# Kernel optimization log

Hardware: AMD Instinct MI355X
Metric: run time of the kernel (lower is better)

## Reference

```python
import jax, jax.numpy as jnp
import numpy as np

N, E, B = 30000, 360000, 8
FN, FE, D, L, M = 64, 16, 128, 3, 8
DK = D // M
NEG_SLOPE = 0.2
EPS = 1e-5


def setup_inputs() -> dict:
    key = jax.random.key(0)
    ks = jax.random.split(key, 24)
    rng = np.random.default_rng(0)
    Ng, Eg = N // B, E // B
    off = np.repeat(np.arange(B, dtype=np.int64) * Ng, Eg)
    src = jnp.asarray(rng.integers(0, Ng, size=E) + off, dtype=jnp.int32)
    dst = jnp.asarray(rng.integers(0, Ng, size=E) + off, dtype=jnp.int32)
    node_graph = jnp.asarray(np.repeat(np.arange(B), Ng), dtype=jnp.int32)
    edge_graph = jnp.asarray(np.repeat(np.arange(B), Eg), dtype=jnp.int32)
    p = lambda i, *s: jax.random.normal(ks[i], s, jnp.float32) * 0.05
    return dict(
        h=jax.random.normal(ks[0], (N, FN), jnp.float32),
        e=jax.random.normal(ks[1], (E, FE), jnp.float32),
        src=src, dst=dst, node_graph=node_graph, edge_graph=edge_graph,
        emb_n_w=p(2, D, FN), emb_n_b=p(3, D),
        emb_e_w=p(4, D, FE), emb_e_b=p(5, D),
        Us=p(6, L, D, D), Vs=p(7, L, D, D), As=p(8, L, D, D),
        Bs=p(9, L, D, D), Cs=p(10, L, D, D),
        gat_src_w=p(11, M * DK, D), gat_src_b=p(12, M * DK),
        gat_dst_w=p(13, M * DK, D), gat_dst_b=p(14, M * DK),
        gat_attn=p(15, M, DK), gat_bias=p(16, M * DK),
        O_w=p(17, D, D), O_b=p(18, D),
        W1_w=p(19, D, 3 * D), W1_b=p(20, D),
        W2_w=p(21, 1, D), W2_b=p(22, 1))


def _bn(x):
    # BatchNorm1d(affine=False), training mode: biased variance over batch dim
    return (x - x.mean(0)) * jax.lax.rsqrt(x.var(0) + EPS)


def reference(h, e, src, dst, node_graph, edge_graph,
              emb_n_w, emb_n_b, emb_e_w, emb_e_b,
              Us, Vs, As, Bs, Cs,
              gat_src_w, gat_src_b, gat_dst_w, gat_dst_b, gat_attn, gat_bias,
              O_w, O_b, W1_w, W1_b, W2_w, W2_b):
    h = h @ emb_n_w.T + emb_n_b  # [N, D]
    e = e @ emb_e_w.T + emb_e_b  # [E, D]
    for l in range(L):
        # u_mul_e('h','w','m') + max('m','agg'): gather-mul-segment_max
        m = (h @ Vs[l].T)[src] * jax.nn.sigmoid(e)  # [E, D]
        agg = jax.ops.segment_max(m, dst, num_segments=N)
        agg = jnp.where(jnp.isneginf(agg), 0.0, agg)  # DGL fills zero-in-degree with 0
        h_new = h + jax.nn.relu(_bn(h @ Us[l].T + agg))
        # inc('in')^T @ B(h) = B(h)[dst]; inc('out')^T @ C(h) = C(h)[src] (uses pre-update h)
        ee = (h @ Bs[l].T)[dst] + (h @ Cs[l].T)[src]
        e = e + jax.nn.relu(_bn(e @ As[l].T + ee))
        h = h_new
    # GATv2Conv(D, DK, M heads, allow_zero_in_degree=True)
    fs = (h @ gat_src_w.T + gat_src_b).reshape(N, M, DK)
    fd = (h @ gat_dst_w.T + gat_dst_b).reshape(N, M, DK)
    z = jax.nn.leaky_relu(fs[src] + fd[dst], NEG_SLOPE)  # [E, M, DK]
    score = jnp.einsum('emk,mk->em', z, gat_attn)        # [E, M]
    smax = jax.ops.segment_max(score, dst, num_segments=N)[dst]
    p = jnp.exp(score - smax)
    denom = jax.ops.segment_sum(p, dst, num_segments=N)[dst]
    a = p / denom
    rst = jax.ops.segment_sum(a[:, :, None] * fs[src], dst, num_segments=N)
    rst = rst + gat_bias.reshape(1, M, DK)
    h = rst.reshape(N, D) @ O_w.T + O_b
    # per-graph mean of node states, broadcast to that graph's edges
    cnt = jax.ops.segment_sum(jnp.ones((N,), h.dtype), node_graph, num_segments=B)
    moy = jax.ops.segment_sum(h, node_graph, num_segments=B) / cnt[:, None]
    out = jnp.concatenate([moy[edge_graph], h[src], h[dst]], axis=1)  # [E, 3D]
    out = jax.nn.relu(out @ W1_w.T + W1_b)
    out = out @ W2_w.T + W2_b
    return jax.nn.sigmoid(out)[:, 0]
```

## Files before the change

kernel.cpp:

```cpp
#include <hip/hip_runtime.h>

#define DF 128
#define NGRAPH 8

typedef __attribute__((ext_vector_type(8))) short bf16x8;
typedef __attribute__((ext_vector_type(4))) float f32x4;

__device__ __forceinline__ float sigm(float x) { return 1.f / (1.f + __expf(-x)); }
__device__ __forceinline__ unsigned short f2bf(float f) {
  unsigned u = __float_as_uint(f);
  u += 0x7FFFu + ((u >> 16) & 1u);
  return (unsigned short)(u >> 16);
}
__device__ __forceinline__ float bf2f(unsigned short u) {
  return __uint_as_float(((unsigned)u) << 16);
}
__device__ __forceinline__ float bflo(unsigned u) { return __uint_as_float(u << 16); }
__device__ __forceinline__ float bfhi(unsigned u) { return __uint_as_float(u & 0xffff0000u); }

__device__ __forceinline__ bf16x8 cvt8(const float* __restrict__ p) {
  float4 a = *(const float4*)p;
  float4 b = *(const float4*)(p + 4);
  bf16x8 r;
  r[0] = (short)f2bf(a.x); r[1] = (short)f2bf(a.y);
  r[2] = (short)f2bf(a.z); r[3] = (short)f2bf(a.w);
  r[4] = (short)f2bf(b.x); r[5] = (short)f2bf(b.y);
  r[6] = (short)f2bf(b.z); r[7] = (short)f2bf(b.w);
  return r;
}

__device__ __forceinline__ void agg_max(unsigned hv, unsigned ev, float& m0, float& m1) {
  m0 = fmaxf(m0, bflo(hv) * sigm(bflo(ev)));
  m1 = fmaxf(m1, bfhi(hv) * sigm(bfhi(ev)));
}

__global__ void k_fill_u32(unsigned* __restrict__ p, unsigned v, long long n) {
  long long i = (long long)blockIdx.x * blockDim.x + threadIdx.x;
  long long st = (long long)gridDim.x * blockDim.x;
  for (; i < n; i += st) p[i] = v;
}

__global__ void k_deg(const int* __restrict__ dst, unsigned* __restrict__ deg, int E) {
  int i = blockIdx.x * blockDim.x + threadIdx.x;
  int st = gridDim.x * blockDim.x;
  for (; i < E; i += st) atomicAdd(&deg[dst[i]], 1u);
}

__global__ __launch_bounds__(1024) void k_scan(
    const unsigned* __restrict__ deg, unsigned* __restrict__ rowptr,
    unsigned* __restrict__ cursor, int N) {
  __shared__ unsigned part[1024];
  int t = threadIdx.x;
  int per = (N + 1023) >> 10;
  int s0 = t * per, s1 = min(N, s0 + per);
  unsigned s = 0;
  for (int i = s0; i < s1; ++i) s += deg[i];
  part[t] = s;
  __syncthreads();
  for (int off = 1; off < 1024; off <<= 1) {
    unsigned v = (t >= off) ? part[t - off] : 0u;
    __syncthreads();
    part[t] += v;
    __syncthreads();
  }
  unsigned base = (t == 0) ? 0u : part[t - 1];
  for (int i = s0; i < s1; ++i) {
    rowptr[i] = base;
    cursor[i] = base;
    base += deg[i];
  }
  if (t == 1023) rowptr[N] = part[1023];
}

__global__ void k_scatter(const int* __restrict__ dst, unsigned* __restrict__ cursor,
                          int* __restrict__ eidb, int E) {
  int i = blockIdx.x * blockDim.x + threadIdx.x;
  int st = gridDim.x * blockDim.x;
  for (; i < E; i += st) {
    unsigned p = atomicAdd(&cursor[dst[i]], 1u);
    eidb[p] = i;
  }
}

__global__ void k_permidx(const int* __restrict__ eidb, const int* __restrict__ src,
                          const int* __restrict__ dst, int* __restrict__ srcP,
                          int* __restrict__ dstP, int E) {
  int i = blockIdx.x * blockDim.x + threadIdx.x;
  int st = gridDim.x * blockDim.x;
  for (; i < E; i += st) {
    int e = eidb[i];
    srcP[i] = src[e];
    dstP[i] = dst[e];
  }
}

__global__ __launch_bounds__(512) void k_wconv(
    const float* __restrict__ Us, const float* __restrict__ Vs,
    const float* __restrict__ As, const float* __restrict__ Bs,
    const float* __restrict__ Cs, const float* __restrict__ gsw,
    const float* __restrict__ gdw, const float* __restrict__ Ow,
    const float* __restrict__ W1, short* __restrict__ out) {
  int b = blockIdx.x;
  const float* W;
  int ldw = DF;
  if (b < 3) W = Us + b * 16384;
  else if (b < 6) W = Vs + (b - 3) * 16384;
  else if (b < 9) W = As + (b - 6) * 16384;
  else if (b < 12) W = Bs + (b - 9) * 16384;
  else if (b < 15) W = Cs + (b - 12) * 16384;
  else if (b == 15) W = gsw;
  else if (b == 16) W = gdw;
  else if (b == 17) W = Ow;
  else if (b == 18) { W = W1 + 128; ldw = 384; }
  else { W = W1 + 256; ldw = 384; }
  short* o = out + (size_t)b * 2048 * 8;
  for (int s = threadIdx.x; s < 2048; s += 512) {
    int ct = s >> 8, ks = (s >> 6) & 3, l = s & 63;
    int row = ct * 16 + (l & 15), k0 = ks * 32 + (l >> 4) * 8;
    *(bf16x8*)&o[s * 8] = cvt8(W + (size_t)row * ldw + k0);
  }
}

__global__ __launch_bounds__(128) void k_node_embed(
    const float* __restrict__ hin, const float* __restrict__ w,
    const float* __restrict__ b, float* __restrict__ h0, int rows) {
  __shared__ float Wt[64 * DF];
  __shared__ float ar[4][64];
  int tid = threadIdx.x;
  for (int i = tid; i < 64 * DF; i += 128) Wt[(i & 63) * DF + (i >> 6)] = w[i];
  float bb = b[tid];
  __syncthreads();
  for (int r0 = blockIdx.x * 4; r0 < rows; r0 += gridDim.x * 4) {
    for (int i = tid; i < 256; i += 128) ar[i >> 6][i & 63] = hin[(size_t)r0 * 64 + i];
    __syncthreads();
    float a0 = bb, a1 = bb, a2 = bb, a3 = bb;
#pragma unroll 8
    for (int k = 0; k < 64; ++k) {
      float wv = Wt[k * DF + tid];
      a0 = fmaf(ar[0][k], wv, a0); a1 = fmaf(ar[1][k], wv, a1);
      a2 = fmaf(ar[2][k], wv, a2); a3 = fmaf(ar[3][k], wv, a3);
    }
    h0[(size_t)r0 * DF + tid] = a0;
    h0[(size_t)(r0 + 1) * DF + tid] = a1;
    h0[(size_t)(r0 + 2) * DF + tid] = a2;
    h0[(size_t)(r0 + 3) * DF + tid] = a3;
    __syncthreads();
  }
}

__global__ __launch_bounds__(128) void k_edge_embed(
    const float* __restrict__ ein, const int* __restrict__ eidb,
    const float* __restrict__ w, const float* __restrict__ b,
    unsigned short* __restrict__ e0u, int rows) {
  __shared__ float Wt[16 * DF];
  __shared__ float ar[4][16];
  int tid = threadIdx.x;
  for (int i = tid; i < 16 * DF; i += 128) Wt[(i & 15) * DF + (i >> 4)] = w[i];
  float bb = b[tid];
  __syncthreads();
  for (int r0 = blockIdx.x * 4; r0 < rows; r0 += gridDim.x * 4) {
    if (tid < 64) {
      int e = eidb[r0 + (tid >> 4)];
      ar[tid >> 4][tid & 15] = ein[(size_t)e * 16 + (tid & 15)];
    }
    __syncthreads();
    float a0 = bb, a1 = bb, a2 = bb, a3 = bb;
#pragma unroll
    for (int k = 0; k < 16; ++k) {
      float wv = Wt[k * DF + tid];
      a0 = fmaf(ar[0][k], wv, a0); a1 = fmaf(ar[1][k], wv, a1);
      a2 = fmaf(ar[2][k], wv, a2); a3 = fmaf(ar[3][k], wv, a3);
    }
    e0u[(size_t)r0 * DF + tid] = f2bf(a0);
    e0u[(size_t)(r0 + 1) * DF + tid] = f2bf(a1);
    e0u[(size_t)(r0 + 2) * DF + tid] = f2bf(a2);
    e0u[(size_t)(r0 + 3) * DF + tid] = f2bf(a3);
    __syncthreads();
  }
}

template <int OUTBF>
__global__ __launch_bounds__(512) void k_gemm_mfma(
    const float* __restrict__ A, const short* __restrict__ Wf,
    const float* __restrict__ bias, void* __restrict__ outv, int rows) {
  __shared__ short Wb[2048 * 8];
  int tid = threadIdx.x;
  for (int s = tid; s < 2048; s += 512)
    *(bf16x8*)&Wb[s * 8] = *(const bf16x8*)&Wf[(size_t)s * 8];
  __syncthreads();
  float* outf = (float*)outv;
  unsigned short* outb = (unsigned short*)outv;
  int wid = tid >> 6, lane = tid & 63, q = lane >> 4, m = lane & 15;
  int ntiles = (rows + 127) >> 7;
  for (int t = blockIdx.x; t < ntiles; t += gridDim.x) {
    int r0 = t * 128 + wid * 16;
    int rr = r0 + m;
    if (rr >= rows) rr = rows - 1;
    const float* ap = A + (size_t)rr * DF + q * 8;
    bf16x8 a[4];
#pragma unroll
    for (int ks = 0; ks < 4; ++ks) a[ks] = cvt8(ap + 32 * ks);
#pragma unroll
    for (int ct = 0; ct < 8; ++ct) {
      f32x4 acc = {0.f, 0.f, 0.f, 0.f};
#pragma unroll
      for (int ks = 0; ks < 4; ++ks) {
        bf16x8 b = *(const bf16x8*)&Wb[((ct * 4 + ks) * 64 + lane) * 8];
        acc = __builtin_amdgcn_mfma_f32_16x16x32_bf16(a[ks], b, acc, 0, 0, 0);
      }
      int col = ct * 16 + m;
      float bb = bias ? bias[col] : 0.f;
#pragma unroll
      for (int j = 0; j < 4; ++j) {
        int row = r0 + q * 4 + j;
        if (row < rows) {
          if (OUTBF) outb[(size_t)row * DF + col] = f2bf(acc[j] + bb);
          else outf[(size_t)row * DF + col] = acc[j] + bb;
        }
      }
    }
  }
}

__global__ __launch_bounds__(512) void k_gemmb_mfma(
    const unsigned short* __restrict__ A, const short* __restrict__ Wf,
    unsigned short* __restrict__ outb, int rows) {
  __shared__ short Wb[2048 * 8];
  int tid = threadIdx.x;
  for (int s = tid; s < 2048; s += 512)
    *(bf16x8*)&Wb[s * 8] = *(const bf16x8*)&Wf[(size_t)s * 8];
  __syncthreads();
  int wid = tid >> 6, lane = tid & 63, q = lane >> 4, m = lane & 15;
  int ntiles = (rows + 127) >> 7;
  for (int t = blockIdx.x; t < ntiles; t += gridDim.x) {
    int r0 = t * 128 + wid * 16;
    int rr = r0 + m;
    if (rr >= rows) rr = rows - 1;
    const unsigned short* ap = A + (size_t)rr * DF + q * 8;
    bf16x8 a[4];
#pragma unroll
    for (int ks = 0; ks < 4; ++ks) a[ks] = *(const bf16x8*)(ap + 32 * ks);
#pragma unroll
    for (int ct = 0; ct < 8; ++ct) {
      f32x4 acc = {0.f, 0.f, 0.f, 0.f};
#pragma unroll
      for (int ks = 0; ks < 4; ++ks) {
        bf16x8 b = *(const bf16x8*)&Wb[((ct * 4 + ks) * 64 + lane) * 8];
        acc = __builtin_amdgcn_mfma_f32_16x16x32_bf16(a[ks], b, acc, 0, 0, 0);
      }
      int col = ct * 16 + m;
#pragma unroll
      for (int j = 0; j < 4; ++j) {
        int row = r0 + q * 4 + j;
        if (row < rows) outb[(size_t)row * DF + col] = f2bf(acc[j]);
      }
    }
  }
}

__global__ __launch_bounds__(512) void k_gemm4_mfma(
    const float* __restrict__ h0, const short* __restrict__ Vf,
    const short* __restrict__ Uf, const short* __restrict__ Bf,
    const short* __restrict__ Cf, unsigned short* __restrict__ hVb,
    float* __restrict__ hU, unsigned short* __restrict__ hBb,
    unsigned short* __restrict__ hCb, int rows) {
  __shared__ short Wl[4 * 2048 * 8];
  int tid = threadIdx.x;
  for (int s = tid; s < 2048; s += 512) {
    *(bf16x8*)&Wl[(size_t)s * 8] = *(const bf16x8*)&Vf[(size_t)s * 8];
    *(bf16x8*)&Wl[(size_t)(2048 + s) * 8] = *(const bf16x8*)&Uf[(size_t)s * 8];
    *(bf16x8*)&Wl[(size_t)(4096 + s) * 8] = *(const bf16x8*)&Bf[(size_t)s * 8];
    *(bf16x8*)&Wl[(size_t)(6144 + s) * 8] = *(const bf16x8*)&Cf[(size_t)s * 8];
  }
  __syncthreads();
  int wid = tid >> 6, lane = tid & 63, q = lane >> 4, m = lane & 15;
  int ntiles = (rows + 127) >> 7;
  for (int t = blockIdx.x; t < ntiles; t += gridDim.x) {
    int r0 = t * 128 + wid * 16;
    int rr = r0 + m;
    if (rr >= rows) rr = rows - 1;
    const float* ap = h0 + (size_t)rr * DF + q * 8;
    bf16x8 a[4];
#pragma unroll
    for (int ks = 0; ks < 4; ++ks) a[ks] = cvt8(ap + 32 * ks);
#pragma unroll
    for (int w = 0; w < 4; ++w) {
#pragma unroll
      for (int ct = 0; ct < 8; ++ct) {
        f32x4 acc = {0.f, 0.f, 0.f, 0.f};
#pragma unroll
        for (int ks = 0; ks < 4; ++ks) {
          bf16x8 b = *(const bf16x8*)&Wl[((w * 2048) + (ct * 4 + ks) * 64 + lane) * 8];
          acc = __builtin_amdgcn_mfma_f32_16x16x32_bf16(a[ks], b, acc, 0, 0, 0);
        }
        int col = ct * 16 + m;
#pragma unroll
        for (int j = 0; j < 4; ++j) {
          int row = r0 + q * 4 + j;
          if (row < rows) {
            if (w == 1) hU[(size_t)row * DF + col] = acc[j];
            else {
              unsigned short v = f2bf(acc[j]);
              unsigned short* o = (w == 0) ? hVb : ((w == 2) ? hBb : hCb);
              o[(size_t)row * DF + col] = v;
            }
          }
        }
      }
    }
  }
}

#define EDGE_MFMA_BODY                                                                 \
  const unsigned short* ep = e0u + (size_t)ec * DF + q * 8;                            \
  bf16x8 bv0 = *(const bf16x8*)(ep);                                                   \
  bf16x8 bv1 = *(const bf16x8*)(ep + 32);                                              \
  bf16x8 bv2 = *(const bf16x8*)(ep + 64);                                              \
  bf16x8 bv3 = *(const bf16x8*)(ep + 96);                                              \
  f32x4 c0 = {0.f, 0.f, 0.f, 0.f}, c1 = c0, c2 = c0, c3 = c0;                          \
  f32x4 c4 = c0, c5 = c0, c6 = c0, c7 = c0;                                            \
  _Pragma("unroll") for (int ks = 0; ks < 4; ++ks) {                                   \
    bf16x8 bv = (ks == 0) ? bv0 : (ks == 1) ? bv1 : (ks == 2) ? bv2 : bv3;             \
    c0 = __builtin_amdgcn_mfma_f32_16x16x32_bf16(*(const bf16x8*)&Wb[((0 * 4 + ks) * 64 + lane) * 8], bv, c0, 0, 0, 0); \
    c1 = __builtin_amdgcn_mfma_f32_16x16x32_bf16(*(const bf16x8*)&Wb[((1 * 4 + ks) * 64 + lane) * 8], bv, c1, 0, 0, 0); \
    c2 = __builtin_amdgcn_mfma_f32_16x16x32_bf16(*(const bf16x8*)&Wb[((2 * 4 + ks) * 64 + lane) * 8], bv, c2, 0, 0, 0); \
    c3 = __builtin_amdgcn_mfma_f32_16x16x32_bf16(*(const bf16x8*)&Wb[((3 * 4 + ks) * 64 + lane) * 8], bv, c3, 0, 0, 0); \
    c4 = __builtin_amdgcn_mfma_f32_16x16x32_bf16(*(const bf16x8*)&Wb[((4 * 4 + ks) * 64 + lane) * 8], bv, c4, 0, 0, 0); \
    c5 = __builtin_amdgcn_mfma_f32_16x16x32_bf16(*(const bf16x8*)&Wb[((5 * 4 + ks) * 64 + lane) * 8], bv, c5, 0, 0, 0); \
    c6 = __builtin_amdgcn_mfma_f32_16x16x32_bf16(*(const bf16x8*)&Wb[((6 * 4 + ks) * 64 + lane) * 8], bv, c6, 0, 0, 0); \
    c7 = __builtin_amdgcn_mfma_f32_16x16x32_bf16(*(const bf16x8*)&Wb[((7 * 4 + ks) * 64 + lane) * 8], bv, c7, 0, 0, 0); \
  }

__global__ __launch_bounds__(512) void k_edge_xs(
    const unsigned short* __restrict__ e0u, const short* __restrict__ Af,
    const unsigned short* __restrict__ hBb, const unsigned short* __restrict__ hCb,
    const int* __restrict__ srcP, const int* __restrict__ dstP,
    float* __restrict__ stat, int Eg) {
  __shared__ short Wb[2048 * 8];
  __shared__ float ls[256];
  int tid = threadIdx.x;
  for (int s = tid; s < 2048; s += 512)
    *(bf16x8*)&Wb[s * 8] = *(const bf16x8*)&Af[(size_t)s * 8];
  if (tid < 256) ls[tid] = 0.f;
  int wid = tid >> 6, lane = tid & 63, q = lane >> 4, m = lane & 15;
  int g = blockIdx.x & 7, sub = blockIdx.x >> 3, nsub = gridDim.x >> 3;
  int gbase = g * Eg, gend = gbase + Eg;
  int tpg = (Eg + 127) >> 7;
  float ps[32], pq[32];
#pragma unroll
  for (int i = 0; i < 32; ++i) { ps[i] = 0.f; pq[i] = 0.f; }
  __syncthreads();
  for (int t = sub; t < tpg; t += nsub) {
    int r0 = gbase + t * 128 + wid * 16;
    int edge = r0 + m;
    bool ok = edge < gend;
    int ec = ok ? edge : gend - 1;
    EDGE_MFMA_BODY
    if (ok) {
      int sidx = srcP[ec], didx = dstP[ec];
      const unsigned short* pb = hBb + (size_t)didx * DF + q * 4;
      const unsigned short* pc = hCb + (size_t)sidx * DF + q * 4;
#pragma unroll
      for (int ct = 0; ct < 8; ++ct) {
        f32x4 cc = (ct == 0) ? c0 : (ct == 1) ? c1 : (ct == 2) ? c2 : (ct == 3) ? c3
                   : (ct == 4) ? c4 : (ct == 5) ? c5 : (ct == 6) ? c6 : c7;
        ushort4 hb = *(const ushort4*)(pb + ct * 16);
        ushort4 hc = *(const ushort4*)(pc + ct * 16);
        float x0 = cc[0] + bf2f(hb.x) + bf2f(hc.x);
        float x1 = cc[1] + bf2f(hb.y) + bf2f(hc.y);
        float x2 = cc[2] + bf2f(hb.z) + bf2f(hc.z);
        float x3 = cc[3] + bf2f(hb.w) + bf2f(hc.w);
        ps[ct * 4 + 0] += x0; pq[ct * 4 + 0] += x0 * x0;
        ps[ct * 4 + 1] += x1; pq[ct * 4 + 1] += x1 * x1;
        ps[ct * 4 + 2] += x2; pq[ct * 4 + 2] += x2 * x2;
        ps[ct * 4 + 3] += x3; pq[ct * 4 + 3] += x3 * x3;
      }
    }
  }
#pragma unroll
  for (int i = 0; i < 32; ++i) {
    float s = ps[i], sq = pq[i];
    s += __shfl_xor(s, 1, 64); sq += __shfl_xor(sq, 1, 64);
    s += __shfl_xor(s, 2, 64); sq += __shfl_xor(sq, 2, 64);
    s += __shfl_xor(s, 4, 64); sq += __shfl_xor(sq, 4, 64);
    s += __shfl_xor(s, 8, 64); sq += __shfl_xor(sq, 8, 64);
    if (m == 0) {
      int feat = (i >> 2) * 16 + q * 4 + (i & 3);
      atomicAdd(&ls[feat], s);
      atomicAdd(&ls[128 + feat], sq);
    }
  }
  __syncthreads();
  if (tid < 128) {
    atomicAdd(&stat[512 + tid], ls[tid]);
    atomicAdd(&stat[640 + tid], ls[128 + tid]);
  }
}

__global__ __launch_bounds__(512) void k_edge_xa(
    unsigned short* __restrict__ e0u, const short* __restrict__ Af,
    const unsigned short* __restrict__ hBb, const unsigned short* __restrict__ hCb,
    const int* __restrict__ srcP, const int* __restrict__ dstP,
    const float* __restrict__ stat, int Eg) {
  __shared__ short Wb[2048 * 8];
  int tid = threadIdx.x;
  for (int s = tid; s < 2048; s += 512)
    *(bf16x8*)&Wb[s * 8] = *(const bf16x8*)&Af[(size_t)s * 8];
  int wid = tid >> 6, lane = tid & 63, q = lane >> 4, m = lane & 15;
  float mm[32], iv[32];
#pragma unroll
  for (int ct = 0; ct < 8; ++ct)
#pragma unroll
    for (int j = 0; j < 4; ++j) {
      int f = ct * 16 + q * 4 + j;
      mm[ct * 4 + j] = stat[768 + f];
      iv[ct * 4 + j] = stat[896 + f];
    }
  int g = blockIdx.x & 7, sub = blockIdx.x >> 3, nsub = gridDim.x >> 3;
  int gbase = g * Eg, gend = gbase + Eg;
  int tpg = (Eg + 127) >> 7;
  __syncthreads();
  for (int t = sub; t < tpg; t += nsub) {
    int r0 = gbase + t * 128 + wid * 16;
    int edge = r0 + m;
    bool ok = edge < gend;
    int ec = ok ? edge : gend - 1;
    EDGE_MFMA_BODY
    if (ok) {
      int sidx = srcP[ec], didx = dstP[ec];
      const unsigned short* pb = hBb + (size_t)didx * DF + q * 4;
      const unsigned short* pc = hCb + (size_t)sidx * DF + q * 4;
      unsigned short* pe = e0u + (size_t)ec * DF + q * 4;
#pragma unroll
      for (int ct = 0; ct < 8; ++ct) {
        f32x4 cc = (ct == 0) ? c0 : (ct == 1) ? c1 : (ct == 2) ? c2 : (ct == 3) ? c3
                   : (ct == 4) ? c4 : (ct == 5) ? c5 : (ct == 6) ? c6 : c7;
        ushort4 hb = *(const ushort4*)(pb + ct * 16);
        ushort4 hc = *(const ushort4*)(pc + ct * 16);
        ushort4 eo = *(const ushort4*)(pe + ct * 16);
        float x0 = cc[0] + bf2f(hb.x) + bf2f(hc.x);
        float x1 = cc[1] + bf2f(hb.y) + bf2f(hc.y);
        float x2 = cc[2] + bf2f(hb.z) + bf2f(hc.z);
        float x3 = cc[3] + bf2f(hb.w) + bf2f(hc.w);
        ushort4 nv;
        nv.x = f2bf(bf2f(eo.x) + fmaxf((x0 - mm[ct * 4 + 0]) * iv[ct * 4 + 0], 0.f));
        nv.y = f2bf(bf2f(eo.y) + fmaxf((x1 - mm[ct * 4 + 1]) * iv[ct * 4 + 1], 0.f));
        nv.z = f2bf(bf2f(eo.z) + fmaxf((x2 - mm[ct * 4 + 2]) * iv[ct * 4 + 2], 0.f));
        nv.w = f2bf(bf2f(eo.w) + fmaxf((x3 - mm[ct * 4 + 3]) * iv[ct * 4 + 3], 0.f));
        *(ushort4*)(pe + ct * 16) = nv;
      }
    }
  }
}

__global__ __launch_bounds__(256) void k_node_agg(
    float* __restrict__ hU, const unsigned short* __restrict__ hVb,
    const unsigned short* __restrict__ e0u, const int* __restrict__ srcP,
    const unsigned* __restrict__ rowptr, float* __restrict__ stat, int Ngr) {
  __shared__ float sr[4][256];
  int tid = threadIdx.x, wid = tid >> 6, lane = tid & 63;
  int g = blockIdx.x & 7, sub = blockIdx.x >> 3, nsub = gridDim.x >> 3;
  float ps0 = 0.f, ps1 = 0.f, pq0 = 0.f, pq1 = 0.f;
  for (int nn = sub * 4 + wid; nn < Ngr; nn += nsub * 4) {
    int n = g * Ngr + nn;
    unsigned r0 = rowptr[n], r1 = rowptr[n + 1];
    float m0 = -3.4e38f, m1 = -3.4e38f;
    for (unsigned rc = r0; rc < r1; rc += 64) {
      int batch = (int)min(64u, r1 - rc);
      int myS = srcP[rc + ((lane < batch) ? lane : 0)];
      int j = 0;
      for (; j + 4 <= batch; j += 4) {
        int s0 = __shfl(myS, j, 64), s1 = __shfl(myS, j + 1, 64);
        int s2 = __shfl(myS, j + 2, 64), s3 = __shfl(myS, j + 3, 64);
        unsigned h0v = *(const unsigned*)&hVb[(size_t)s0 * DF + 2 * lane];
        unsigned h1v = *(const unsigned*)&hVb[(size_t)s1 * DF + 2 * lane];
        unsigned h2v = *(const unsigned*)&hVb[(size_t)s2 * DF + 2 * lane];
        unsigned h3v = *(const unsigned*)&hVb[(size_t)s3 * DF + 2 * lane];
        unsigned v0 = *(const unsigned*)&e0u[(size_t)(rc + j) * DF + 2 * lane];
        unsigned v1 = *(const unsigned*)&e0u[(size_t)(rc + j + 1) * DF + 2 * lane];
        unsigned v2 = *(const unsigned*)&e0u[(size_t)(rc + j + 2) * DF + 2 * lane];
        unsigned v3 = *(const unsigned*)&e0u[(size_t)(rc + j + 3) * DF + 2 * lane];
        agg_max(h0v, v0, m0, m1);
        agg_max(h1v, v1, m0, m1);
        agg_max(h2v, v2, m0, m1);
        agg_max(h3v, v3, m0, m1);
      }
      for (; j < batch; ++j) {
        int s = __shfl(myS, j, 64);
        unsigned hv = *(const unsigned*)&hVb[(size_t)s * DF + 2 * lane];
        unsigned ev = *(const unsigned*)&e0u[(size_t)(rc + j) * DF + 2 * lane];
        agg_max(hv, ev, m0, m1);
      }
    }
    if (r1 == r0) { m0 = 0.f; m1 = 0.f; }
    size_t idx = (size_t)n * DF + 2 * lane;
    float2 hu = *(float2*)&hU[idx];
    float t0 = hu.x + m0, t1 = hu.y + m1;
    hu.x = t0; hu.y = t1;
    *(float2*)&hU[idx] = hu;
    ps0 += t0; ps1 += t1;
    pq0 += t0 * t0; pq1 += t1 * t1;
  }
  sr[0][tid] = ps0; sr[1][tid] = ps1; sr[2][tid] = pq0; sr[3][tid] = pq1;
  __syncthreads();
  if (tid < 64) {
    float a0 = 0.f, a1 = 0.f, b0 = 0.f, b1 = 0.f;
#pragma unroll
    for (int w = 0; w < 4; ++w) {
      a0 += sr[0][w * 64 + tid]; a1 += sr[1][w * 64 + tid];
      b0 += sr[2][w * 64 + tid]; b1 += sr[3][w * 64 + tid];
    }
    atomicAdd(&stat[2 * tid], a0);
    atomicAdd(&stat[2 * tid + 1], a1);
    atomicAdd(&stat[128 + 2 * tid], b0);
    atomicAdd(&stat[128 + 2 * tid + 1], b1);
  }
}

__global__ void k_bn_finalize(float* __restrict__ stat, float nN, float nE) {
  int tid = threadIdx.x;
  if (tid < 128) {
    float mean = stat[tid] / nN;
    float var = stat[128 + tid] / nN - mean * mean;
    stat[256 + tid] = mean;
    stat[384 + tid] = rsqrtf(fmaxf(var, 0.f) + 1e-5f);
  } else {
    int d = tid - 128;
    float mean = stat[512 + d] / nE;
    float var = stat[640 + d] / nE - mean * mean;
    stat[768 + d] = mean;
    stat[896 + d] = rsqrtf(fmaxf(var, 0.f) + 1e-5f);
  }
}

__global__ __launch_bounds__(256) void k_node_update(
    float* __restrict__ h0, const float* __restrict__ hU,
    const float* __restrict__ stat, long long total) {
  long long i = (long long)blockIdx.x * blockDim.x + threadIdx.x;
  long long st = (long long)gridDim.x * blockDim.x;
  for (; i < total; i += st) {
    int d = (int)(i & 127);
    float t = (hU[i] - stat[256 + d]) * stat[384 + d];
    h0[i] += fmaxf(t, 0.f);
  }
}

__global__ __launch_bounds__(256) void k_gat_score(
    const unsigned short* __restrict__ fsb, const unsigned short* __restrict__ fdb,
    const int* __restrict__ srcP, const int* __restrict__ dstP,
    const float* __restrict__ attn, float* __restrict__ score, int E) {
  long long i = (long long)blockIdx.x * blockDim.x + threadIdx.x;
  long long st = (long long)gridDim.x * blockDim.x;
  long long total = (long long)E * 8;
  for (; i < total; i += st) {
    int e = (int)(i >> 3), mh = (int)(i & 7);
    int s = srcP[e], dn = dstP[e];
    const unsigned short* ps = fsb + (size_t)s * DF + mh * 16;
    const unsigned short* pd = fdb + (size_t)dn * DF + mh * 16;
    const float* pa = attn + mh * 16;
    bf16x8 s0 = *(const bf16x8*)ps;
    bf16x8 s1 = *(const bf16x8*)(ps + 8);
    bf16x8 d0 = *(const bf16x8*)pd;
    bf16x8 d1 = *(const bf16x8*)(pd + 8);
    float acc = 0.f;
#pragma unroll
    for (int kk = 0; kk < 8; ++kk) {
      float z = bf2f((unsigned short)s0[kk]) + bf2f((unsigned short)d0[kk]);
      z = (z > 0.f) ? z : 0.2f * z;
      acc = fmaf(z, pa[kk], acc);
      float z2 = bf2f((unsigned short)s1[kk]) + bf2f((unsigned short)d1[kk]);
      z2 = (z2 > 0.f) ? z2 : 0.2f * z2;
      acc = fmaf(z2, pa[kk + 8], acc);
    }
    score[i] = acc;
  }
}

__global__ __launch_bounds__(256) void k_gat_node(
    const float* __restrict__ score, const unsigned short* __restrict__ fsb,
    const int* __restrict__ srcP, const unsigned* __restrict__ rowptr,
    float* __restrict__ rst, int Ngr) {
  int tid = threadIdx.x, wid = tid >> 6, lane = tid & 63;
  int g = blockIdx.x & 7, sub = blockIdx.x >> 3, nsub = gridDim.x >> 3;
  int head = lane >> 3, slot = lane & 7;
  for (int nn = sub * 4 + wid; nn < Ngr; nn += nsub * 4) {
    int n = g * Ngr + nn;
    unsigned r0 = rowptr[n], r1 = rowptr[n + 1];
    float hm = -3.4e38f;
    for (unsigned r = r0 + slot; r < r1; r += 8)
      hm = fmaxf(hm, score[(size_t)r * 8 + head]);
#pragma unroll
    for (int mk = 1; mk < 8; mk <<= 1) hm = fmaxf(hm, __shfl_xor(hm, mk, 64));
    float dn = 0.f;
    for (unsigned r = r0 + slot; r < r1; r += 8)
      dn += __expf(score[(size_t)r * 8 + head] - hm);
#pragma unroll
    for (int mk = 1; mk < 8; mk <<= 1) dn += __shfl_xor(dn, mk, 64);
    float inv = (r1 > r0) ? 1.f / dn : 0.f;
    float a0 = 0.f, a1 = 0.f;
    for (unsigned rc = r0; rc < r1; rc += 64) {
      int batch = (int)min(64u, r1 - rc);
      int myS = srcP[rc + ((lane < batch) ? lane : 0)];
      int j = 0;
      for (; j + 4 <= batch; j += 4) {
        int s0 = __shfl(myS, j, 64), s1 = __shfl(myS, j + 1, 64);
        int s2 = __shfl(myS, j + 2, 64), s3 = __shfl(myS, j + 3, 64);
        float sc0 = score[(size_t)(rc + j) * 8 + head];
        float sc1 = score[(size_t)(rc + j + 1) * 8 + head];
        float sc2 = score[(size_t)(rc + j + 2) * 8 + head];
        float sc3 = score[(size_t)(rc + j + 3) * 8 + head];
        unsigned f0 = *(const unsigned*)&fsb[(size_t)s0 * DF + 2 * lane];
        unsigned f1 = *(const unsigned*)&fsb[(size_t)s1 * DF + 2 * lane];
        unsigned f2 = *(const unsigned*)&fsb[(size_t)s2 * DF + 2 * lane];
        unsigned f3 = *(const unsigned*)&fsb[(size_t)s3 * DF + 2 * lane];
        float w0 = __expf(sc0 - hm) * inv, w1 = __expf(sc1 - hm) * inv;
        float w2 = __expf(sc2 - hm) * inv, w3 = __expf(sc3 - hm) * inv;
        a0 = fmaf(w0, bflo(f0), a0); a1 = fmaf(w0, bfhi(f0), a1);
        a0 = fmaf(w1, bflo(f1), a0); a1 = fmaf(w1, bfhi(f1), a1);
        a0 = fmaf(w2, bflo(f2), a0); a1 = fmaf(w2, bfhi(f2), a1);
        a0 = fmaf(w3, bflo(f3), a0); a1 = fmaf(w3, bfhi(f3), a1);
      }
      for (; j < batch; ++j) {
        int s = __shfl(myS, j, 64);
        float w = __expf(score[(size_t)(rc + j) * 8 + head] - hm) * inv;
        unsigned fv = *(const unsigned*)&fsb[(size_t)s * DF + 2 * lane];
        a0 = fmaf(w, bflo(fv), a0);
        a1 = fmaf(w, bfhi(fv), a1);
      }
    }
    float2 o;
    o.x = a0; o.y = a1;
    *(float2*)&rst[(size_t)n * DF + 2 * lane] = o;
  }
}

__global__ void k_bias2(const float* __restrict__ gat_bias,
                        const float* __restrict__ O_w,
                        const float* __restrict__ O_b, float* __restrict__ bias2) {
  int d = threadIdx.x;
  float acc = O_b[d];
  for (int k = 0; k < DF; ++k) acc = fmaf(gat_bias[k], O_w[(size_t)d * DF + k], acc);
  bias2[d] = acc;
}

__global__ __launch_bounds__(128) void k_moy(
    const unsigned short* __restrict__ h2b, const int* __restrict__ ng,
    float* __restrict__ moy, float* __restrict__ cnt, int rows) {
  int tid = threadIdx.x;
  int per = (rows + gridDim.x - 1) / gridDim.x;
  int n0 = blockIdx.x * per;
  int n1 = min(rows, n0 + per);
  if (n0 >= n1) return;
  int cur = ng[n0];
  float acc = 0.f; int c = 0;
  for (int n = n0; n < n1; ++n) {
    int g = ng[n];
    if (g != cur) {
      atomicAdd(&moy[cur * DF + tid], acc);
      if (tid == 0) atomicAdd(&cnt[cur], (float)c);
      acc = 0.f; c = 0; cur = g;
    }
    acc += bf2f(h2b[(size_t)n * DF + tid]);
    ++c;
  }
  atomicAdd(&moy[cur * DF + tid], acc);
  if (tid == 0) atomicAdd(&cnt[cur], (float)c);
}

__global__ void k_p0(const float* __restrict__ W1, const float* __restrict__ W1b_,
                     const float* __restrict__ moy, const float* __restrict__ cnt,
                     float* __restrict__ P0) {
  int g = blockIdx.x, d = threadIdx.x;
  float inv = 1.f / cnt[g];
  float acc = W1b_[d];
  for (int k = 0; k < DF; ++k) acc = fmaf(W1[(size_t)d * 384 + k], moy[g * DF + k] * inv, acc);
  P0[g * DF + d] = acc;
}

__global__ __launch_bounds__(256) void k_head(
    const unsigned short* __restrict__ P1b, const unsigned short* __restrict__ P2b,
    const float* __restrict__ P0, const int* __restrict__ srcP,
    const unsigned* __restrict__ rowptr, const int* __restrict__ eidb,
    const float* __restrict__ W2, const float* __restrict__ W2b,
    float* __restrict__ out, int Ngr) {
  int tid = threadIdx.x, wid = tid >> 6, lane = tid & 63;
  int g = blockIdx.x & 7, sub = blockIdx.x >> 3, nsub = gridDim.x >> 3;
  float w2b = W2b[0];
  float w20 = W2[2 * lane], w21 = W2[2 * lane + 1];
  float b0 = P0[g * DF + 2 * lane], b1v = P0[g * DF + 2 * lane + 1];
  for (int nn = sub * 4 + wid; nn < Ngr; nn += nsub * 4) {
    int n = g * Ngr + nn;
    unsigned r0 = rowptr[n], r1 = rowptr[n + 1];
    if (r1 == r0) continue;
    unsigned p2 = *(const unsigned*)&P2b[(size_t)n * DF + 2 * lane];
    float base0 = b0 + bflo(p2);
    float base1 = b1v + bfhi(p2);
    for (unsigned rc = r0; rc < r1; rc += 64) {
      int cnt2 = (int)min(64u, r1 - rc);
      int myE = eidb[rc + ((lane < cnt2) ? lane : 0)];
      int myS = srcP[rc + ((lane < cnt2) ? lane : 0)];
      int j = 0;
      for (; j + 4 <= cnt2; j += 4) {
        int e0 = __shfl(myE, j, 64), e1 = __shfl(myE, j + 1, 64);
        int e2 = __shfl(myE, j + 2, 64), e3 = __shfl(myE, j + 3, 64);
        int s0 = __shfl(myS, j, 64), s1 = __shfl(myS, j + 1, 64);
        int s2 = __shfl(myS, j + 2, 64), s3 = __shfl(myS, j + 3, 64);
        unsigned u0 = *(const unsigned*)&P1b[(size_t)s0 * DF + 2 * lane];
        unsigned u1 = *(const unsigned*)&P1b[(size_t)s1 * DF + 2 * lane];
        unsigned u2 = *(const unsigned*)&P1b[(size_t)s2 * DF + 2 * lane];
        unsigned u3 = *(const unsigned*)&P1b[(size_t)s3 * DF + 2 * lane];
        float v0 = fmaxf(base0 + bflo(u0), 0.f) * w20 + fmaxf(base1 + bfhi(u0), 0.f) * w21;
        float v1 = fmaxf(base0 + bflo(u1), 0.f) * w20 + fmaxf(base1 + bfhi(u1), 0.f) * w21;
        float v2 = fmaxf(base0 + bflo(u2), 0.f) * w20 + fmaxf(base1 + bfhi(u2), 0.f) * w21;
        float v3 = fmaxf(base0 + bflo(u3), 0.f) * w20 + fmaxf(base1 + bfhi(u3), 0.f) * w21;
#pragma unroll
        for (int mk = 1; mk < 64; mk <<= 1) {
          v0 += __shfl_xor(v0, mk, 64);
          v1 += __shfl_xor(v1, mk, 64);
          v2 += __shfl_xor(v2, mk, 64);
          v3 += __shfl_xor(v3, mk, 64);
        }
        if (lane == 0) {
          out[e0] = sigm(v0 + w2b);
          out[e1] = sigm(v1 + w2b);
          out[e2] = sigm(v2 + w2b);
          out[e3] = sigm(v3 + w2b);
        }
      }
      for (; j < cnt2; ++j) {
        int e = __shfl(myE, j, 64);
        int s = __shfl(myS, j, 64);
        unsigned p1 = *(const unsigned*)&P1b[(size_t)s * DF + 2 * lane];
        float v = fmaxf(base0 + bflo(p1), 0.f) * w20 + fmaxf(base1 + bfhi(p1), 0.f) * w21;
#pragma unroll
        for (int mk = 1; mk < 64; mk <<= 1) v += __shfl_xor(v, mk, 64);
        if (lane == 0) out[e] = sigm(v + w2b);
      }
    }
  }
}

extern "C" void kernel_launch(void* const* d_in, const int* in_sizes, int n_in,
                              void* d_out, int out_size, void* d_ws, size_t ws_size,
                              hipStream_t stream) {
  const float* h_in = (const float*)d_in[0];
  const float* e_in = (const float*)d_in[1];
  const int* src = (const int*)d_in[2];
  const int* dst = (const int*)d_in[3];
  const int* node_graph = (const int*)d_in[4];
  const float* emb_n_w = (const float*)d_in[6];
  const float* emb_n_b = (const float*)d_in[7];
  const float* emb_e_w = (const float*)d_in[8];
  const float* emb_e_b = (const float*)d_in[9];
  const float* Us = (const float*)d_in[10];
  const float* Vs = (const float*)d_in[11];
  const float* As = (const float*)d_in[12];
  const float* Bs = (const float*)d_in[13];
  const float* Cs = (const float*)d_in[14];
  const float* gat_src_w = (const float*)d_in[15];
  const float* gat_src_b = (const float*)d_in[16];
  const float* gat_dst_w = (const float*)d_in[17];
  const float* gat_dst_b = (const float*)d_in[18];
  const float* gat_attn = (const float*)d_in[19];
  const float* gat_bias = (const float*)d_in[20];
  const float* O_w = (const float*)d_in[21];
  const float* O_b = (const float*)d_in[22];
  const float* W1_w = (const float*)d_in[23];
  const float* W1_b = (const float*)d_in[24];
  const float* W2_w = (const float*)d_in[25];
  const float* W2_b = (const float*)d_in[26];
  float* out = (float*)d_out;

  const int N = in_sizes[0] / 64;
  const int E = in_sizes[1] / 16;
  const int Eg = E / NGRAPH;
  const int Ngr = N / NGRAPH;

  auto rnd = [](size_t b) { return (b + 255) & ~(size_t)255; };
  const size_t sz_e0 = rnd((size_t)E * DF * 2);
  const size_t sz_node = rnd((size_t)N * DF * 4);
  const size_t sz_nodeb = rnd((size_t)N * DF * 2);
  const size_t sz_score = rnd((size_t)E * 8 * 4);
  const size_t sz_wfrag = rnd(20 * 2048 * 8 * 2);
  const size_t sz_rp = rnd((size_t)(N + 1) * 4);
  const size_t sz_eid = rnd((size_t)E * 4);
  const size_t sz_misc = rnd(4096 * 4);
  const size_t needed = sz_e0 + 3 * sz_node + 4 * sz_nodeb + sz_score + sz_wfrag +
                        3 * sz_rp + 3 * sz_eid + sz_misc;
  if (ws_size < needed) {
    k_fill_u32<<<256, 256, 0, stream>>>((unsigned*)out, 0xBF800000u, (long long)out_size);
    return;
  }

  char* wp = (char*)d_ws;
  auto alloc = [&](size_t bytes) { void* p = wp; wp += bytes; return p; };
  unsigned short* e0u = (unsigned short*)alloc(sz_e0);
  float* h0 = (float*)alloc(sz_node);
  float* hU = (float*)alloc(sz_node);
  float* rst = (float*)alloc(sz_node);
  unsigned short* hVb = (unsigned short*)alloc(sz_nodeb);
  unsigned short* hBb = (unsigned short*)alloc(sz_nodeb);
  unsigned short* hCb = (unsigned short*)alloc(sz_nodeb);
  unsigned short* h2b = (unsigned short*)alloc(sz_nodeb);
  float* score = (float*)alloc(sz_score);
  short* wfrag = (short*)alloc(sz_wfrag);
  unsigned* rowptr = (unsigned*)alloc(sz_rp);
  unsigned* cursor = (unsigned*)alloc(sz_rp);
  unsigned* deg = (unsigned*)alloc(sz_rp);
  int* eidb = (int*)alloc(sz_eid);
  int* srcP = (int*)alloc(sz_eid);
  int* dstP = (int*)alloc(sz_eid);
  float* misc = (float*)alloc(sz_misc);
  float* stat = misc;
  float* bias2 = misc + 1024;
  float* moy = misc + 1152;
  float* cnt = misc + 2176;
  float* P0 = misc + 2304;
  unsigned short* P1b = e0u;
  unsigned short* P2b = e0u + (size_t)N * DF;

  auto WF = [&](int idx) { return wfrag + (size_t)idx * 2048 * 8; };

  k_fill_u32<<<64, 256, 0, stream>>>(deg, 0u, N);
  k_deg<<<512, 256, 0, stream>>>(dst, deg, E);
  k_scan<<<1, 1024, 0, stream>>>(deg, rowptr, cursor, N);
  k_scatter<<<512, 256, 0, stream>>>(dst, cursor, eidb, E);
  k_permidx<<<512, 256, 0, stream>>>(eidb, src, dst, srcP, dstP, E);

  k_wconv<<<20, 512, 0, stream>>>(Us, Vs, As, Bs, Cs, gat_src_w, gat_dst_w, O_w,
                                  W1_w, wfrag);

  const int gN = (N + 127) / 128;
  k_node_embed<<<2048, 128, 0, stream>>>(h_in, emb_n_w, emb_n_b, h0, N);
  k_edge_embed<<<4096, 128, 0, stream>>>(e_in, eidb, emb_e_w, emb_e_b, e0u, E);

  for (int l = 0; l < 3; ++l) {
    k_gemm4_mfma<<<gN, 512, 0, stream>>>(h0, WF(3 + l), WF(l), WF(9 + l), WF(12 + l),
                                         hVb, hU, hBb, hCb, N);
    k_fill_u32<<<4, 256, 0, stream>>>((unsigned*)stat, 0u, 1024);
    k_node_agg<<<2048, 256, 0, stream>>>(hU, hVb, e0u, srcP, rowptr, stat, Ngr);
    k_edge_xs<<<1024, 512, 0, stream>>>(e0u, WF(6 + l), hBb, hCb, srcP, dstP, stat, Eg);
    k_bn_finalize<<<1, 256, 0, stream>>>(stat, (float)N, (float)E);
    k_node_update<<<2048, 256, 0, stream>>>(h0, hU, stat, (long long)N * DF);
    k_edge_xa<<<1024, 512, 0, stream>>>(e0u, WF(6 + l), hBb, hCb, srcP, dstP, stat, Eg);
  }

  k_gemm_mfma<1><<<gN, 512, 0, stream>>>(h0, WF(15), gat_src_b, hVb, N);
  k_gemm_mfma<1><<<gN, 512, 0, stream>>>(h0, WF(16), gat_dst_b, hBb, N);
  k_gat_score<<<2048, 256, 0, stream>>>(hVb, hBb, srcP, dstP, gat_attn, score, E);
  k_gat_node<<<2048, 256, 0, stream>>>(score, hVb, srcP, rowptr, rst, Ngr);
  k_bias2<<<1, 128, 0, stream>>>(gat_bias, O_w, O_b, bias2);
  k_gemm_mfma<1><<<gN, 512, 0, stream>>>(rst, WF(17), bias2, h2b, N);

  k_fill_u32<<<2, 256, 0, stream>>>((unsigned*)moy, 0u, 1032);
  k_moy<<<128, 128, 0, stream>>>(h2b, node_graph, moy, cnt, N);
  k_p0<<<8, 128, 0, stream>>>(W1_w, W1_b, moy, cnt, P0);
  k_gemmb_mfma<<<gN, 512, 0, stream>>>(h2b, WF(18), P1b, N);
  k_gemmb_mfma<<<gN, 512, 0, stream>>>(h2b, WF(19), P2b, N);
  k_head<<<2048, 256, 0, stream>>>(P1b, P2b, P0, srcP, rowptr, eidb, W2_w, W2_b,
                                   out, Ngr);
}
```

Baseline: 1.388 ms.

## Replace per-node max aggregation with edge-window scan and ordered-int atomicMax

The per-node pull over the CSR is replaced by an edge-parallel kernel. Each wavefront scans a fixed window of 64 dst-sorted edges, keeps a running max per destination, and flushes each segment to a global buffer with atomicMax on an order-preserving integer encoding of floats. A separate kernel then decodes the maxima, maps empty segments to zero, adds them into hU and accumulates the BatchNorm statistics. The intent is to balance work regardless of node degree. The cost is an extra fill and an extra full pass over node-sized buffers, plus global atomics at segment boundaries.

```diff
diff --git a/kernel.cpp b/kernel.cpp
--- a/kernel.cpp
+++ b/kernel.cpp
@@ -6,6 +6,16 @@
 typedef __attribute__((ext_vector_type(8))) short bf16x8;
 typedef __attribute__((ext_vector_type(4))) float f32x4;
 
+constexpr unsigned ENC_NEGINF = 0x007FFFFFu;
+
+__device__ __forceinline__ unsigned enc_f(float f) {
+  unsigned u = __float_as_uint(f);
+  return (u & 0x80000000u) ? ~u : (u | 0x80000000u);
+}
+__device__ __forceinline__ float dec_f(unsigned k) {
+  unsigned u = (k & 0x80000000u) ? (k & 0x7FFFFFFFu) : ~k;
+  return __uint_as_float(u);
+}
 __device__ __forceinline__ float sigm(float x) { return 1.f / (1.f + __expf(-x)); }
 __device__ __forceinline__ unsigned short f2bf(float f) {
   unsigned u = __float_as_uint(f);
@@ -27,11 +37,6 @@
   r[4] = (short)f2bf(b.x); r[5] = (short)f2bf(b.y);
   r[6] = (short)f2bf(b.z); r[7] = (short)f2bf(b.w);
   return r;
-}
-
-__device__ __forceinline__ void agg_max(unsigned hv, unsigned ev, float& m0, float& m1) {
-  m0 = fmaxf(m0, bflo(hv) * sigm(bflo(ev)));
-  m1 = fmaxf(m1, bfhi(hv) * sigm(bfhi(ev)));
 }
 
 __global__ void k_fill_u32(unsigned* __restrict__ p, unsigned v, long long n) {
@@ -453,67 +458,92 @@
   }
 }
 
-__global__ __launch_bounds__(256) void k_node_agg(
-    float* __restrict__ hU, const unsigned short* __restrict__ hVb,
-    const unsigned short* __restrict__ e0u, const int* __restrict__ srcP,
-    const unsigned* __restrict__ rowptr, float* __restrict__ stat, int Ngr) {
-  __shared__ float sr[4][256];
+#define FLUSH_MAX()                                                        \
+  {                                                                        \
+    atomicMax(&agg[(size_t)curD * DF + 2 * lane], enc_f(m0));              \
+    atomicMax(&agg[(size_t)curD * DF + 2 * lane + 1], enc_f(m1));          \
+    m0 = -3.4e38f; m1 = -3.4e38f;                                          \
+  }
+
+__global__ __launch_bounds__(256) void k_edge_max2(
+    const unsigned short* __restrict__ hVb, const unsigned short* __restrict__ e0u,
+    const int* __restrict__ srcP, const int* __restrict__ dstP,
+    unsigned* __restrict__ agg, int Eg) {
   int tid = threadIdx.x, wid = tid >> 6, lane = tid & 63;
   int g = blockIdx.x & 7, sub = blockIdx.x >> 3, nsub = gridDim.x >> 3;
-  float ps0 = 0.f, ps1 = 0.f, pq0 = 0.f, pq1 = 0.f;
-  for (int nn = sub * 4 + wid; nn < Ngr; nn += nsub * 4) {
-    int n = g * Ngr + nn;
-    unsigned r0 = rowptr[n], r1 = rowptr[n + 1];
+  int gbase = g * Eg;
+  int nwin = (Eg + 63) >> 6;
+  for (int w = sub * 4 + wid; w < nwin; w += nsub * 4) {
+    int base = gbase + (w << 6);
+    int cnt = min(64, gbase + Eg - base);
+    int li = base + ((lane < cnt) ? lane : cnt - 1);
+    int myS = srcP[li];
+    int myD = dstP[li];
+    int curD = __shfl(myD, 0, 64);
     float m0 = -3.4e38f, m1 = -3.4e38f;
-    for (unsigned rc = r0; rc < r1; rc += 64) {
-      int batch = (int)min(64u, r1 - rc);
-      int myS = srcP[rc + ((lane < batch) ? lane : 0)];
-      int j = 0;
-      for (; j + 4 <= batch; j += 4) {
-        int s0 = __shfl(myS, j, 64), s1 = __shfl(myS, j + 1, 64);
-        int s2 = __shfl(myS, j + 2, 64), s3 = __shfl(myS, j + 3, 64);
-        unsigned h0v = *(const unsigned*)&hVb[(size_t)s0 * DF + 2 * lane];
-        unsigned h1v = *(const unsigned*)&hVb[(size_t)s1 * DF + 2 * lane];
-        unsigned h2v = *(const unsigned*)&hVb[(size_t)s2 * DF + 2 * lane];
-        unsigned h3v = *(const unsigned*)&hVb[(size_t)s3 * DF + 2 * lane];
-        unsigned v0 = *(const unsigned*)&e0u[(size_t)(rc + j) * DF + 2 * lane];
-        unsigned v1 = *(const unsigned*)&e0u[(size_t)(rc + j + 1) * DF + 2 * lane];
-        unsigned v2 = *(const unsigned*)&e0u[(size_t)(rc + j + 2) * DF + 2 * lane];
-        unsigned v3 = *(const unsigned*)&e0u[(size_t)(rc + j + 3) * DF + 2 * lane];
-        agg_max(h0v, v0, m0, m1);
-        agg_max(h1v, v1, m0, m1);
-        agg_max(h2v, v2, m0, m1);
-        agg_max(h3v, v3, m0, m1);
-      }
-      for (; j < batch; ++j) {
-        int s = __shfl(myS, j, 64);
-        unsigned hv = *(const unsigned*)&hVb[(size_t)s * DF + 2 * lane];
-        unsigned ev = *(const unsigned*)&e0u[(size_t)(rc + j) * DF + 2 * lane];
-        agg_max(hv, ev, m0, m1);
-      }
-    }
-    if (r1 == r0) { m0 = 0.f; m1 = 0.f; }
-    size_t idx = (size_t)n * DF + 2 * lane;
-    float2 hu = *(float2*)&hU[idx];
-    float t0 = hu.x + m0, t1 = hu.y + m1;
-    hu.x = t0; hu.y = t1;
-    *(float2*)&hU[idx] = hu;
-    ps0 += t0; ps1 += t1;
-    pq0 += t0 * t0; pq1 += t1 * t1;
-  }
-  sr[0][tid] = ps0; sr[1][tid] = ps1; sr[2][tid] = pq0; sr[3][tid] = pq1;
-  __syncthreads();
-  if (tid < 64) {
-    float a0 = 0.f, a1 = 0.f, b0 = 0.f, b1 = 0.f;
-#pragma unroll
-    for (int w = 0; w < 4; ++w) {
-      a0 += sr[0][w * 64 + tid]; a1 += sr[1][w * 64 + tid];
-      b0 += sr[2][w * 64 + tid]; b1 += sr[3][w * 64 + tid];
-    }
-    atomicAdd(&stat[2 * tid], a0);
-    atomicAdd(&stat[2 * tid + 1], a1);
-    atomicAdd(&stat[128 + 2 * tid], b0);
-    atomicAdd(&stat[128 + 2 * tid + 1], b1);
+    int j = 0;
+    for (; j + 4 <= cnt; j += 4) {
+      int s0 = __shfl(myS, j, 64), s1 = __shfl(myS, j + 1, 64);
+      int s2 = __shfl(myS, j + 2, 64), s3 = __shfl(myS, j + 3, 64);
+      int d0 = __shfl(myD, j, 64), d1 = __shfl(myD, j + 1, 64);
+      int d2 = __shfl(myD, j + 2, 64), d3 = __shfl(myD, j + 3, 64);
+      unsigned h0 = *(const unsigned*)&hVb[(size_t)s0 * DF + 2 * lane];
+      unsigned h1 = *(const unsigned*)&hVb[(size_t)s1 * DF + 2 * lane];
+      unsigned h2 = *(const unsigned*)&hVb[(size_t)s2 * DF + 2 * lane];
+      unsigned h3 = *(const unsigned*)&hVb[(size_t)s3 * DF + 2 * lane];
+      unsigned v0 = *(const unsigned*)&e0u[(size_t)(base + j) * DF + 2 * lane];
+      unsigned v1 = *(const unsigned*)&e0u[(size_t)(base + j + 1) * DF + 2 * lane];
+      unsigned v2 = *(const unsigned*)&e0u[(size_t)(base + j + 2) * DF + 2 * lane];
+      unsigned v3 = *(const unsigned*)&e0u[(size_t)(base + j + 3) * DF + 2 * lane];
+      float a0 = bflo(h0) * sigm(bflo(v0)), b0 = bfhi(h0) * sigm(bfhi(v0));
+      float a1 = bflo(h1) * sigm(bflo(v1)), b1 = bfhi(h1) * sigm(bfhi(v1));
+      float a2 = bflo(h2) * sigm(bflo(v2)), b2 = bfhi(h2) * sigm(bfhi(v2));
+      float a3 = bflo(h3) * sigm(bflo(v3)), b3 = bfhi(h3) * sigm(bfhi(v3));
+      if (d0 != curD) { FLUSH_MAX(); curD = d0; }
+      m0 = fmaxf(m0, a0); m1 = fmaxf(m1, b0);
+      if (d1 != curD) { FLUSH_MAX(); curD = d1; }
+      m0 = fmaxf(m0, a1); m1 = fmaxf(m1, b1);
+      if (d2 != curD) { FLUSH_MAX(); curD = d2; }
+      m0 = fmaxf(m0, a2); m1 = fmaxf(m1, b2);
+      if (d3 != curD) { FLUSH_MAX(); curD = d3; }
+      m0 = fmaxf(m0, a3); m1 = fmaxf(m1, b3);
+    }
+    for (; j < cnt; ++j) {
+      int s = __shfl(myS, j, 64);
+      int d = __shfl(myD, j, 64);
+      unsigned hv = *(const unsigned*)&hVb[(size_t)s * DF + 2 * lane];
+      unsigned ev = *(const unsigned*)&e0u[(size_t)(base + j) * DF + 2 * lane];
+      float a = bflo(hv) * sigm(bflo(ev)), b = bfhi(hv) * sigm(bfhi(ev));
+      if (d != curD) { FLUSH_MAX(); curD = d; }
+      m0 = fmaxf(m0, a); m1 = fmaxf(m1, b);
+    }
+    atomicMax(&agg[(size_t)curD * DF + 2 * lane], enc_f(m0));
+    atomicMax(&agg[(size_t)curD * DF + 2 * lane + 1], enc_f(m1));
+  }
+}
+
+__global__ __launch_bounds__(256) void k_node_fin(
+    float* __restrict__ hU, const unsigned* __restrict__ agg,
+    float* __restrict__ stat, long long total) {
+  __shared__ float ls[512];
+  int tid = threadIdx.x;
+  float ps = 0.f, pq = 0.f;
+  long long i = (long long)blockIdx.x * 256 + tid;
+  long long st = (long long)gridDim.x * 256;
+  for (; i < total; i += st) {
+    unsigned k = agg[i];
+    float a = (k == ENC_NEGINF) ? 0.f : dec_f(k);
+    float t = hU[i] + a;
+    hU[i] = t;
+    ps += t;
+    pq += t * t;
+  }
+  ls[tid] = ps;
+  ls[256 + tid] = pq;
+  __syncthreads();
+  if (tid < 128) {
+    atomicAdd(&stat[tid], ls[tid] + ls[tid + 128]);
+    atomicAdd(&stat[128 + tid], ls[256 + tid] + ls[256 + tid + 128]);
   }
 }
 
@@ -818,6 +848,7 @@
   float* P0 = misc + 2304;
   unsigned short* P1b = e0u;
   unsigned short* P2b = e0u + (size_t)N * DF;
+  unsigned* agg = (unsigned*)rst;
 
   auto WF = [&](int idx) { return wfrag + (size_t)idx * 2048 * 8; };
 
@@ -837,8 +868,10 @@
   for (int l = 0; l < 3; ++l) {
     k_gemm4_mfma<<<gN, 512, 0, stream>>>(h0, WF(3 + l), WF(l), WF(9 + l), WF(12 + l),
                                          hVb, hU, hBb, hCb, N);
+    k_fill_u32<<<1024, 256, 0, stream>>>(agg, ENC_NEGINF, (long long)N * DF);
     k_fill_u32<<<4, 256, 0, stream>>>((unsigned*)stat, 0u, 1024);
-    k_node_agg<<<2048, 256, 0, stream>>>(hU, hVb, e0u, srcP, rowptr, stat, Ngr);
+    k_edge_max2<<<1024, 256, 0, stream>>>(hVb, e0u, srcP, dstP, agg, Eg);
+    k_node_fin<<<1024, 256, 0, stream>>>(hU, agg, stat, (long long)N * DF);
     k_edge_xs<<<1024, 512, 0, stream>>>(e0u, WF(6 + l), hBb, hCb, srcP, dstP, stat, Eg);
     k_bn_finalize<<<1, 256, 0, stream>>>(stat, (float)N, (float)E);
     k_node_update<<<2048, 256, 0, stream>>>(h0, hU, stat, (long long)N * DF);
```

New measurement: 1.268 ms, median of 2. 8.7% less time.
